# Kernel tuning notes

Measured on AMD Instinct MI355X. Metric: run time of the kernel, lower is better.

The kernel has to match this reference:

```python
import jax, jax.numpy as jnp
import numpy as np

D_MODEL = 512
WINDOW_SIZE = 257


def setup_inputs() -> dict:
    key = jax.random.key(0)
    ks = jax.random.split(key, 7)
    B, S, D = 4, 4096, D_MODEL
    scale = 1.0 / np.sqrt(D)
    return {
        "x": jax.random.normal(ks[0], (B, S, D), dtype=jnp.float32),
        "Wq": jax.random.normal(ks[1], (D, D), dtype=jnp.float32) * scale,
        "bq": jnp.zeros((D,), dtype=jnp.float32),
        "Wk": jax.random.normal(ks[2], (D, D), dtype=jnp.float32) * scale,
        "bk": jnp.zeros((D,), dtype=jnp.float32),
        "Wv": jax.random.normal(ks[3], (D, D), dtype=jnp.float32) * scale,
        "bv": jnp.zeros((D,), dtype=jnp.float32),
    }


def reference(x, Wq, bq, Wk, bk, Wv, bv):
    B, S, D = x.shape
    half_window = (WINDOW_SIZE - 1) // 2
    Q = x @ Wq + bq
    K = x @ Wk + bk
    V = x @ Wv + bv
    # full [B,S,S] scores, then band mask |i-j| <= half_window (matches original)
    scores = jnp.einsum("bsd,btd->bst", Q, K) / jnp.sqrt(jnp.asarray(D, x.dtype))
    idx = jnp.arange(S)
    local_mask = jnp.abs(idx[:, None] - idx[None, :]) <= half_window  # [S,S]
    scores = jnp.where(local_mask[None], scores, -jnp.inf)
    attn = jax.nn.softmax(scores, axis=-1)
    return jnp.einsum("bst,btd->bsd", attn, V)
```

## Files before the change

### kernel.cpp

```cpp
#include <hip/hip_runtime.h>
#include <hip/hip_bf16.h>

#define S_LEN   4096
#define D_MOD   512
#define BATCH   4
#define HALF_W  128
#define M_TOT   (BATCH * S_LEN)

typedef __attribute__((ext_vector_type(8))) short bf16x8;
typedef __attribute__((ext_vector_type(4))) float f32x4;

__device__ __forceinline__ unsigned short f2bf(float f) {
    unsigned int u = __float_as_uint(f);
    unsigned int r = (u + 0x7fffu + ((u >> 16) & 1u)) >> 16;
    return (unsigned short)r;
}

__device__ __forceinline__ void async_copy16(const void* g, void* l) {
    __builtin_amdgcn_global_load_lds(
        (const __attribute__((address_space(1))) void*)g,
        (__attribute__((address_space(3))) void*)l, 16, 0, 0);
}

__global__ __launch_bounds__(256) void convert_xw(const float* __restrict__ x,
                                                  const float* __restrict__ Wq,
                                                  const float* __restrict__ Wk,
                                                  const float* __restrict__ Wv,
                                                  unsigned short* __restrict__ xb,
                                                  unsigned short* __restrict__ Wt) {
    __shared__ float sT[64][65];
    const int t = threadIdx.x;
    const int bid = blockIdx.x;
    if (bid < 8192) {
        int i = (bid * 256 + t) * 4;
        float4 v = *(const float4*)(x + i);
        ushort4 o;
        o.x = f2bf(v.x); o.y = f2bf(v.y); o.z = f2bf(v.z); o.w = f2bf(v.w);
        *(ushort4*)(xb + i) = o;
        return;
    }
    const int j = bid - 8192;
    const int w = j >> 6;
    const int rj = j & 63;
    const float* W = (w == 0) ? Wq : ((w == 1) ? Wk : Wv);
    const int n0 = (rj & 7) * 64, k0 = (rj >> 3) * 64;
    const int r = t >> 4, c4 = (t & 15) * 4;
    #pragma unroll
    for (int i = 0; i < 4; ++i) {
        float4 v = *(const float4*)(W + (size_t)(k0 + r + i * 16) * 512 + n0 + c4);
        sT[c4 + 0][r + i * 16] = v.x;
        sT[c4 + 1][r + i * 16] = v.y;
        sT[c4 + 2][r + i * 16] = v.z;
        sT[c4 + 3][r + i * 16] = v.w;
    }
    __syncthreads();
    #pragma unroll
    for (int i = 0; i < 4; ++i) {
        int rr = (t >> 4) + i * 16;
        ushort4 o;
        o.x = f2bf(sT[rr][c4 + 0]);
        o.y = f2bf(sT[rr][c4 + 1]);
        o.z = f2bf(sT[rr][c4 + 2]);
        o.w = f2bf(sT[rr][c4 + 3]);
        *(ushort4*)(Wt + (size_t)w * 262144 + (size_t)(n0 + rr) * 512 + k0 + c4) = o;
    }
}

__global__ __launch_bounds__(256) void qkv_gemm(
    const unsigned short* __restrict__ xb, const unsigned short* __restrict__ Wt,
    const float* __restrict__ bq, const float* __restrict__ bk, const float* __restrict__ bv,
    unsigned short* __restrict__ Qo, unsigned short* __restrict__ Ko,
    unsigned short* __restrict__ Vt) {
    __shared__ __align__(16) char gsmem[34816];
    unsigned short* sA = (unsigned short*)gsmem;
    unsigned short* sB = (unsigned short*)(gsmem + 16384);
    unsigned short* sT = (unsigned short*)gsmem;

    const int t = threadIdx.x;
    const int p = blockIdx.x;
    const int l = (p & 7) * 192 + (p >> 3);
    const int mi = l / 12;
    const int rzn = l - mi * 12;
    const int wsel = rzn >> 2;
    const int ni = rzn & 3;
    const int m0 = mi * 128;
    const int n0 = ni * 128;
    const unsigned short* Wb = Wt + (size_t)wsel * 262144;

    const int w = t >> 6, lane = t & 63;
    const int wm = (w & 1) * 64, wn = (w >> 1) * 64;
    const int qd = lane >> 4, l16 = lane & 15;

    f32x4 acc[4][4] = {};

    for (int k0 = 0; k0 < 512; k0 += 64) {
        __syncthreads();
        #pragma unroll
        for (int i = 0; i < 4; ++i) {
            int c = i * 256 + t;
            int row = c >> 3, cc = c & 7;
            int g = cc ^ (row & 7);
            async_copy16(xb + (size_t)(m0 + row) * 512 + k0 + g * 8, sA + c * 8);
            async_copy16(Wb + (size_t)(n0 + row) * 512 + k0 + g * 8, sB + c * 8);
        }
        __syncthreads();
        #pragma unroll
        for (int ks = 0; ks < 2; ++ks) {
            bf16x8 af[4], bfr[4];
            #pragma unroll
            for (int i = 0; i < 4; ++i) {
                int row = wm + i * 16 + l16;
                int ch = (ks * 4 + qd) ^ (row & 7);
                af[i] = *(const bf16x8*)(sA + row * 64 + ch * 8);
            }
            #pragma unroll
            for (int j = 0; j < 4; ++j) {
                int row = wn + j * 16 + l16;
                int ch = (ks * 4 + qd) ^ (row & 7);
                bfr[j] = *(const bf16x8*)(sB + row * 64 + ch * 8);
            }
            #pragma unroll
            for (int i = 0; i < 4; ++i)
                #pragma unroll
                for (int j = 0; j < 4; ++j)
                    acc[i][j] = __builtin_amdgcn_mfma_f32_16x16x32_bf16(af[i], bfr[j], acc[i][j], 0, 0, 0);
        }
    }

    const float* bias = (wsel == 0) ? bq : ((wsel == 1) ? bk : bv);
    __syncthreads();

    if (wsel < 2) {
        #pragma unroll
        for (int j = 0; j < 4; ++j) {
            int n = wn + j * 16 + l16;
            float bj = bias[n0 + n];
            #pragma unroll
            for (int i = 0; i < 4; ++i) {
                int mb = wm + i * 16 + qd * 4;
                #pragma unroll
                for (int r = 0; r < 4; ++r)
                    sT[(mb + r) * 136 + n] = f2bf(acc[i][j][r] + bj);
            }
        }
        __syncthreads();
        unsigned short* Og = (wsel == 0) ? Qo : Ko;
        #pragma unroll
        for (int i2 = 0; i2 < 4; ++i2)
            #pragma unroll
            for (int i3 = 0; i3 < 2; ++i3) {
                int m = i2 * 32 + (t >> 3);
                int ch = (t & 7) + i3 * 8;
                bf16x8 v = *(const bf16x8*)(sT + m * 136 + ch * 8);
                *(bf16x8*)(Og + (size_t)(m0 + m) * 512 + n0 + ch * 8) = v;
            }
    } else {
        #pragma unroll
        for (int j = 0; j < 4; ++j) {
            int n = wn + j * 16 + l16;
            float bj = bias[n0 + n];
            #pragma unroll
            for (int i = 0; i < 4; ++i) {
                int mb = wm + i * 16 + qd * 4;
                #pragma unroll
                for (int r = 0; r < 4; ++r)
                    sT[n * 136 + mb + r] = f2bf(acc[i][j][r] + bj);
            }
        }
        __syncthreads();
        #pragma unroll
        for (int i2 = 0; i2 < 4; ++i2)
            #pragma unroll
            for (int i3 = 0; i3 < 2; ++i3) {
                int n = i2 * 32 + (t >> 3);
                int ch = (t & 7) + i3 * 8;
                bf16x8 v = *(const bf16x8*)(sT + n * 136 + ch * 8);
                *(bf16x8*)(Vt + (size_t)(n0 + n) * M_TOT + m0 + ch * 8) = v;
            }
    }
}

__global__ __launch_bounds__(256) void attn(const unsigned short* __restrict__ Qg,
                                            const unsigned short* __restrict__ Kg,
                                            const unsigned short* __restrict__ Vt,
                                            float* __restrict__ out) {
    __shared__ __align__(16) unsigned short sQ[32 * 520];
    __shared__ __align__(16) unsigned short sKV[32 * 520];
    __shared__ __align__(16) unsigned short sP[32 * 40];
    __shared__ float lsum[32];

    const int t = threadIdx.x;
    const int p = blockIdx.x;
    const int l = (p & 7) * 64 + (p >> 3);
    const int q0 = (l & 127) * 32;
    const int b = l >> 7;
    const int bS = b * S_LEN;
    const int w = t >> 6, lane = t & 63;
    const int qd = lane >> 4, l16 = lane & 15;
    const int qh = (w >> 1) * 16, kh = (w & 1) * 16;

    if (t < 32) lsum[t] = 0.f;

    #pragma unroll
    for (int i = 0; i < 8; ++i) {
        int c = i * 256 + t;
        int row = c >> 6, cc = c & 63;
        async_copy16(Qg + (bS + q0 + row) * 512 + cc * 8, sQ + row * 520 + cc * 8);
    }

    f32x4 oacc[16] = {};

    for (int kt = 0; kt < 9; ++kt) {
        int key0 = q0 - HALF_W + kt * 32;
        if (key0 + 32 <= 0 || key0 >= S_LEN) continue;

        __syncthreads();
        #pragma unroll
        for (int i = 0; i < 8; ++i) {
            int c = i * 256 + t;
            int row = c >> 6, cc = c & 63;
            int rowg = key0 + row;
            rowg = (rowg < 0) ? 0 : ((rowg > S_LEN - 1) ? S_LEN - 1 : rowg);
            async_copy16(Kg + (bS + rowg) * 512 + cc * 8, sKV + row * 520 + cc * 8);
        }
        __syncthreads();

        f32x4 sacc = {0.f, 0.f, 0.f, 0.f};
        #pragma unroll
        for (int c4 = 0; c4 < 4; ++c4) {
            #pragma unroll
            for (int kc = 0; kc < 4; ++kc) {
                bf16x8 aq = *(const bf16x8*)(sQ + (qh + l16) * 520 + c4 * 128 + kc * 32 + qd * 8);
                bf16x8 bk8 = *(const bf16x8*)(sKV + (kh + l16) * 520 + c4 * 128 + kc * 32 + qd * 8);
                sacc = __builtin_amdgcn_mfma_f32_16x16x32_bf16(aq, bk8, sacc, 0, 0, 0);
            }
        }

        const float scale = 0.04419417382415922f;
        #pragma unroll
        for (int r = 0; r < 4; ++r) {
            int qi = q0 + qh + qd * 4 + r;
            int kj = key0 + kh + l16;
            bool valid = (kj >= 0) && (kj < S_LEN) && (kj >= qi - HALF_W) && (kj <= qi + HALF_W);
            float p2 = valid ? __expf(sacc[r] * scale) : 0.f;
            sP[(qh + qd * 4 + r) * 40 + kh + l16] = f2bf(p2);
            float s = p2;
            s += __shfl_xor(s, 1);
            s += __shfl_xor(s, 2);
            s += __shfl_xor(s, 4);
            s += __shfl_xor(s, 8);
            if (l16 == 0) atomicAdd(&lsum[qh + qd * 4 + r], s);
        }

        __syncthreads();
        #pragma unroll
        for (int i = 0; i < 8; ++i) {
            int c = i * 256 + t;
            int row = c >> 2, cc = c & 3;
            int kk = key0 + cc * 8;
            int koff = (kk >= 0 && kk + 8 <= S_LEN) ? kk : 0;
            async_copy16(Vt + (size_t)row * M_TOT + bS + koff, sKV + c * 8);
        }
        __syncthreads();

        #pragma unroll
        for (int c4 = 0; c4 < 4; ++c4) {
            #pragma unroll
            for (int qt = 0; qt < 2; ++qt) {
                bf16x8 ap = *(const bf16x8*)(sP + (qt * 16 + l16) * 40 + qd * 8);
                #pragma unroll
                for (int dt = 0; dt < 2; ++dt) {
                    bf16x8 bv8 = *(const bf16x8*)(sKV + (c4 * 128 + w * 32 + dt * 16 + l16) * 32 + qd * 8);
                    oacc[c4 * 4 + qt * 2 + dt] =
                        __builtin_amdgcn_mfma_f32_16x16x32_bf16(ap, bv8, oacc[c4 * 4 + qt * 2 + dt], 0, 0, 0);
                }
            }
        }
    }

    __syncthreads();
    #pragma unroll
    for (int c4 = 0; c4 < 4; ++c4)
        #pragma unroll
        for (int qt = 0; qt < 2; ++qt)
            #pragma unroll
            for (int dt = 0; dt < 2; ++dt) {
                int dv = c4 * 128 + w * 32 + dt * 16 + l16;
                #pragma unroll
                for (int r = 0; r < 4; ++r) {
                    int q = qt * 16 + qd * 4 + r;
                    out[(size_t)(bS + q0 + q) * 512 + dv] = oacc[c4 * 4 + qt * 2 + dt][r] / lsum[q];
                }
            }
}

extern "C" void kernel_launch(void* const* d_in, const int* in_sizes, int n_in,
                              void* d_out, int out_size, void* d_ws, size_t ws_size,
                              hipStream_t stream) {
    const float* x  = (const float*)d_in[0];
    const float* Wq = (const float*)d_in[1];
    const float* bq = (const float*)d_in[2];
    const float* Wk = (const float*)d_in[3];
    const float* bk = (const float*)d_in[4];
    const float* Wv = (const float*)d_in[5];
    const float* bv = (const float*)d_in[6];
    float* out = (float*)d_out;

    char* ws = (char*)d_ws;
    unsigned short* xb = (unsigned short*)(ws);
    unsigned short* Wt = (unsigned short*)(ws + 16777216);
    unsigned short* Qb = (unsigned short*)(ws + 18350080);
    unsigned short* Kb = (unsigned short*)(ws + 35127296);
    unsigned short* Vt = (unsigned short*)(ws + 51904512);

    convert_xw<<<8384, 256, 0, stream>>>(x, Wq, Wk, Wv, xb, Wt);
    qkv_gemm<<<1536, 256, 0, stream>>>(xb, Wt, bq, bk, bv, Qb, Kb, Vt);
    attn<<<512, 256, 0, stream>>>(Qb, Kb, Vt, out);
}
```

Before: 166.3 us.

## Register-prefetch K/V tiles with swizzled V layout and precomputed inverse sums

Replaces the synchronous global-to-LDS async copies of K and V with loads into registers. The next K tile and the current V tile are fetched while the score and PV MFMAs run, then written to LDS after raw s_barrier calls. The transposed-V LDS layout gains an XOR swizzle to cut bank conflicts, and the loop bounds are computed up front instead of skipping tiles inside the loop. The final normalization now multiplies by precomputed reciprocals instead of dividing per element. The cost is higher register pressure from holding 16 bf16x8 vectors per thread, plus hand-managed waitcnt/barrier ordering that could be fragile.

```diff
diff --git a/kernel.cpp b/kernel.cpp
--- a/kernel.cpp
+++ b/kernel.cpp
@@ -207,30 +207,62 @@
         int row = c >> 6, cc = c & 63;
         async_copy16(Qg + (bS + q0 + row) * 512 + cc * 8, sQ + row * 520 + cc * 8);
     }
-
-    f32x4 oacc[16] = {};
-
-    for (int kt = 0; kt < 9; ++kt) {
-        int key0 = q0 - HALF_W + kt * 32;
-        if (key0 + 32 <= 0 || key0 >= S_LEN) continue;
-
-        __syncthreads();
+    asm volatile("s_waitcnt vmcnt(0)" ::: "memory");
+
+    const int kt_lo = (q0 < 128) ? ((128 - q0) >> 5) : 0;
+    int kt_hi = (4192 - q0) >> 5;
+    if (kt_hi > 8) kt_hi = 8;
+
+    bf16x8 kreg[8], vreg[8];
+
+    {
+        int key0 = q0 - HALF_W + kt_lo * 32;
         #pragma unroll
         for (int i = 0; i < 8; ++i) {
             int c = i * 256 + t;
             int row = c >> 6, cc = c & 63;
             int rowg = key0 + row;
             rowg = (rowg < 0) ? 0 : ((rowg > S_LEN - 1) ? S_LEN - 1 : rowg);
-            async_copy16(Kg + (bS + rowg) * 512 + cc * 8, sKV + row * 520 + cc * 8);
-        }
-        __syncthreads();
+            kreg[i] = *(const bf16x8*)(Kg + (size_t)(bS + rowg) * 512 + cc * 8);
+        }
+    }
+
+    f32x4 oacc[16] = {};
+
+    for (int kt = kt_lo; kt <= kt_hi; ++kt) {
+        const int key0 = q0 - HALF_W + kt * 32;
+
+        asm volatile("s_waitcnt lgkmcnt(0)" ::: "memory");
+        __builtin_amdgcn_s_barrier();
+
+        #pragma unroll
+        for (int i = 0; i < 8; ++i) {
+            int c = i * 256 + t;
+            int row = c >> 6, cc = c & 63;
+            *(bf16x8*)(sKV + row * 520 + cc * 8) = kreg[i];
+        }
+
+        #pragma unroll
+        for (int i = 0; i < 8; ++i) {
+            int c = i * 256 + t;
+            int rp = c >> 3, chs = c & 7;
+            int ch = chs ^ (rp & 7);
+            int d = rp * 2 + (ch >> 2);
+            int kc = ch & 3;
+            int kk = key0 + kc * 8;
+            int koff = (kk >= 0 && kk + 8 <= S_LEN) ? kk : 0;
+            vreg[i] = *(const bf16x8*)(Vt + (size_t)d * M_TOT + bS + koff);
+        }
+
+        asm volatile("s_waitcnt lgkmcnt(0)" ::: "memory");
+        __builtin_amdgcn_s_barrier();
 
         f32x4 sacc = {0.f, 0.f, 0.f, 0.f};
         #pragma unroll
         for (int c4 = 0; c4 < 4; ++c4) {
             #pragma unroll
             for (int kc = 0; kc < 4; ++kc) {
-                bf16x8 aq = *(const bf16x8*)(sQ + (qh + l16) * 520 + c4 * 128 + kc * 32 + qd * 8);
+                bf16x8 aq  = *(const bf16x8*)(sQ  + (qh + l16) * 520 + c4 * 128 + kc * 32 + qd * 8);
                 bf16x8 bk8 = *(const bf16x8*)(sKV + (kh + l16) * 520 + c4 * 128 + kc * 32 + qd * 8);
                 sacc = __builtin_amdgcn_mfma_f32_16x16x32_bf16(aq, bk8, sacc, 0, 0, 0);
             }
@@ -252,16 +284,29 @@
             if (l16 == 0) atomicAdd(&lsum[qh + qd * 4 + r], s);
         }
 
-        __syncthreads();
+        asm volatile("s_waitcnt lgkmcnt(0)" ::: "memory");
+        __builtin_amdgcn_s_barrier();
+
         #pragma unroll
         for (int i = 0; i < 8; ++i) {
             int c = i * 256 + t;
-            int row = c >> 2, cc = c & 3;
-            int kk = key0 + cc * 8;
-            int koff = (kk >= 0 && kk + 8 <= S_LEN) ? kk : 0;
-            async_copy16(Vt + (size_t)row * M_TOT + bS + koff, sKV + c * 8);
-        }
-        __syncthreads();
+            *(bf16x8*)(sKV + c * 8) = vreg[i];
+        }
+
+        if (kt < kt_hi) {
+            int key0n = key0 + 32;
+            #pragma unroll
+            for (int i = 0; i < 8; ++i) {
+                int c = i * 256 + t;
+                int row = c >> 6, cc = c & 63;
+                int rowg = key0n + row;
+                rowg = (rowg < 0) ? 0 : ((rowg > S_LEN - 1) ? S_LEN - 1 : rowg);
+                kreg[i] = *(const bf16x8*)(Kg + (size_t)(bS + rowg) * 512 + cc * 8);
+            }
+        }
+
+        asm volatile("s_waitcnt lgkmcnt(0)" ::: "memory");
+        __builtin_amdgcn_s_barrier();
 
         #pragma unroll
         for (int c4 = 0; c4 < 4; ++c4) {
@@ -270,7 +315,10 @@
                 bf16x8 ap = *(const bf16x8*)(sP + (qt * 16 + l16) * 40 + qd * 8);
                 #pragma unroll
                 for (int dt = 0; dt < 2; ++dt) {
-                    bf16x8 bv8 = *(const bf16x8*)(sKV + (c4 * 128 + w * 32 + dt * 16 + l16) * 32 + qd * 8);
+                    int dv = c4 * 128 + w * 32 + dt * 16 + l16;
+                    int rp = dv >> 1;
+                    int chs = (((dv & 1) << 2) + qd) ^ (rp & 7);
+                    bf16x8 bv8 = *(const bf16x8*)(sKV + rp * 64 + chs * 8);
                     oacc[c4 * 4 + qt * 2 + dt] =
                         __builtin_amdgcn_mfma_f32_16x16x32_bf16(ap, bv8, oacc[c4 * 4 + qt * 2 + dt], 0, 0, 0);
                 }
@@ -278,7 +326,16 @@
         }
     }
 
-    __syncthreads();
+    asm volatile("s_waitcnt lgkmcnt(0)" ::: "memory");
+    __builtin_amdgcn_s_barrier();
+
+    float inv[2][4];
+    #pragma unroll
+    for (int qt = 0; qt < 2; ++qt)
+        #pragma unroll
+        for (int r = 0; r < 4; ++r)
+            inv[qt][r] = 1.0f / lsum[qt * 16 + qd * 4 + r];
+
     #pragma unroll
     for (int c4 = 0; c4 < 4; ++c4)
         #pragma unroll
@@ -289,7 +346,7 @@
                 #pragma unroll
                 for (int r = 0; r < 4; ++r) {
                     int q = qt * 16 + qd * 4 + r;
-                    out[(size_t)(bS + q0 + q) * 512 + dv] = oacc[c4 * 4 + qt * 2 + dt][r] / lsum[q];
+                    out[(size_t)(bS + q0 + q) * 512 + dv] = oacc[c4 * 4 + qt * 2 + dt][r] * inv[qt][r];
                 }
             }
 }
```

Result: no change. 165.1 us (-0.7%).
